# Optimization experiments

Measured on AMD Instinct MI355X. Metric: run time of the kernel, lower is better.

Reference implementation:

```python
import jax, jax.numpy as jnp
import numpy as np

D_MODEL = 512
D_STATE = 16
D_CONV = 4
EXPAND = 2
HEADDIM = 64
D_INNER = EXPAND * D_MODEL            # 1024
NHEADS = D_INNER // HEADDIM           # 16
CONV_DIM = D_INNER + 2 * D_STATE      # 1056 (x, B, C channels)
D_IN_PROJ = 2 * D_INNER + 2 * D_STATE + NHEADS  # 2096
EPS = 1e-5
B_SZ, L_SEQ = 8, 4096


def _mamba_param_keys(prefix):
    return [prefix + n for n in
            ('in_proj', 'conv_w', 'conv_b', 'dt_bias', 'A_log', 'D', 'norm_w', 'out_proj')]


def _make_mamba_params(key, prefix):
    ks = jax.random.split(key, 4)
    s = 0.02
    return {
        prefix + 'in_proj': jax.random.normal(ks[0], (D_IN_PROJ, D_MODEL), jnp.float32) * s,
        prefix + 'conv_w': jax.random.normal(ks[1], (CONV_DIM, D_CONV), jnp.float32) * s,
        prefix + 'conv_b': jnp.zeros((CONV_DIM,), jnp.float32),
        prefix + 'dt_bias': jax.random.normal(ks[2], (NHEADS,), jnp.float32) * 0.1,
        prefix + 'A_log': jnp.log(jnp.arange(1, NHEADS + 1, dtype=jnp.float32)),
        prefix + 'D': jnp.ones((NHEADS,), jnp.float32),
        prefix + 'norm_w': jnp.ones((D_INNER,), jnp.float32),
        prefix + 'out_proj': jax.random.normal(ks[3], (D_MODEL, D_INNER), jnp.float32) * s,
    }


def setup_inputs() -> dict:
    key = jax.random.key(0)
    kx, kf, kb, kp = jax.random.split(key, 4)
    inp = {'x': jax.random.normal(kx, (B_SZ, L_SEQ, D_MODEL), jnp.float32)}
    inp.update(_make_mamba_params(kf, 'f_'))
    inp.update(_make_mamba_params(kb, 'b_'))
    kp1, kp2 = jax.random.split(kp)
    inp['proj_w'] = jax.random.normal(kp1, (D_MODEL, 2 * D_MODEL), jnp.float32) * 0.02
    inp['proj_b'] = jnp.zeros((D_MODEL,), jnp.float32)
    inp['ln_w'] = jnp.ones((D_MODEL,), jnp.float32)
    inp['ln_b'] = jnp.zeros((D_MODEL,), jnp.float32)
    return inp


def mamba2(x, in_proj, conv_w, conv_b, dt_bias, A_log, Dp, norm_w, out_proj):
    """Mamba2 block (ngroups=1): in_proj -> causal depthwise conv -> selective scan -> gated RMSNorm -> out_proj."""
    B, L, _ = x.shape
    zxbcdt = x @ in_proj.T                               # [B,L,2096]
    z = zxbcdt[..., :D_INNER]                            # gate
    xBC = zxbcdt[..., D_INNER:D_INNER + CONV_DIM]
    dt = jax.nn.softplus(zxbcdt[..., D_INNER + CONV_DIM:] + dt_bias)  # [B,L,H]
    # causal depthwise conv over (x, B, C) channels + SiLU
    xp = jnp.pad(xBC, ((0, 0), (D_CONV - 1, 0), (0, 0)))
    conv = conv_b + sum(xp[:, k:k + L, :] * conv_w[:, k] for k in range(D_CONV))
    xBC = jax.nn.silu(conv)
    xs = xBC[..., :D_INNER].reshape(B, L, NHEADS, HEADDIM)  # [B,L,H,P]
    Bm = xBC[..., D_INNER:D_INNER + D_STATE]                # [B,L,N]
    Cm = xBC[..., D_INNER + D_STATE:]                       # [B,L,N]
    A = -jnp.exp(A_log)                                     # [H]
    dA = jnp.exp(dt * A)                                    # [B,L,H]

    def step(h, inp):
        dA_t, dt_t, x_t, B_t, C_t = inp                     # [B,H],[B,H],[B,H,P],[B,N],[B,N]
        h = h * dA_t[..., None, None] + (dt_t[..., None] * x_t)[..., None] * B_t[:, None, None, :]
        y = jnp.einsum('bhpn,bn->bhp', h, C_t)
        return h, y

    h0 = jnp.zeros((B, NHEADS, HEADDIM, D_STATE), x.dtype)
    inps = (dA.transpose(1, 0, 2), dt.transpose(1, 0, 2), xs.transpose(1, 0, 2, 3),
            Bm.transpose(1, 0, 2), Cm.transpose(1, 0, 2))
    _, ys = jax.lax.scan(step, h0, inps)                    # ys: [L,B,H,P]
    y = ys.transpose(1, 0, 2, 3) + Dp[:, None] * xs         # skip connection
    y = y.reshape(B, L, D_INNER)
    # gated RMSNorm (norm_before_gate=False)
    y = y * jax.nn.silu(z)
    y = y * jax.lax.rsqrt(jnp.mean(y * y, axis=-1, keepdims=True) + EPS) * norm_w
    return y @ out_proj.T


def _layer_norm(x, w, b):
    mu = jnp.mean(x, axis=-1, keepdims=True)
    v = jnp.var(x, axis=-1, keepdims=True)
    return (x - mu) * jax.lax.rsqrt(v + EPS) * w + b


def reference(x,
              f_in_proj, f_conv_w, f_conv_b, f_dt_bias, f_A_log, f_D, f_norm_w, f_out_proj,
              b_in_proj, b_conv_w, b_conv_b, b_dt_bias, b_A_log, b_D, b_norm_w, b_out_proj,
              proj_w, proj_b, ln_w, ln_b):
    x_fwd = mamba2(x, f_in_proj, f_conv_w, f_conv_b, f_dt_bias, f_A_log, f_D, f_norm_w, f_out_proj)
    x_bwd = jnp.flip(
        mamba2(jnp.flip(x, axis=1), b_in_proj, b_conv_w, b_conv_b, b_dt_bias, b_A_log, b_D, b_norm_w, b_out_proj),
        axis=1)
    comb = jnp.concatenate([x_fwd, x_bwd], axis=-1)         # [B,L,2D]
    out = comb @ proj_w.T + proj_b                          # dropout is identity (eval / p=0)
    return _layer_norm(x + out, ln_w, ln_b)
```

## Files before the change

### kernel.cpp

```cpp
#include <hip/hip_runtime.h>
#include <hip/hip_bf16.h>
#include <math.h>

typedef __bf16 bf16x8_t __attribute__((ext_vector_type(8)));
typedef float f32x4_t __attribute__((ext_vector_type(4)));
typedef unsigned short u16x8_t __attribute__((ext_vector_type(8)));
typedef unsigned short u16x4_t __attribute__((ext_vector_type(4)));

#define DEV __device__ __forceinline__

DEV float bf2f(unsigned short u) {
    unsigned int v = ((unsigned int)u) << 16;
    return __builtin_bit_cast(float, v);
}
DEV unsigned short f2bf(float f) {
    unsigned int u = __builtin_bit_cast(unsigned int, f);
    u += 0x7fffu + ((u >> 16) & 1u);
    return (unsigned short)(u >> 16);
}

__global__ __launch_bounds__(256) void cvt_k(
    const float* __restrict__ in, unsigned short* __restrict__ out, int n8)
{
    int t = blockIdx.x * 256 + threadIdx.x;
    if (t >= n8) return;
    f32x4_t a = ((const f32x4_t*)in)[t * 2];
    f32x4_t b = ((const f32x4_t*)in)[t * 2 + 1];
    u16x8_t o;
#pragma unroll
    for (int j = 0; j < 4; j++) { o[j] = f2bf(a[j]); o[4 + j] = f2bf(b[j]); }
    ((u16x8_t*)out)[t] = o;
}

template <int NT, bool FLIP_A, bool FLIP_C, bool OUT_F32, bool ADD_BIAS, bool ACCUM>
__global__ __launch_bounds__(256, 2) void gemm_bt(
    const unsigned short* __restrict__ A,
    const unsigned short* __restrict__ W,
    void* __restrict__ Cout,
    const float* __restrict__ bias,
    int N, int K, int ldc, int col_ofs)
{
    __shared__ __attribute__((aligned(16))) unsigned char smem[32768];
    const int tid  = threadIdx.x;
    const int wave = tid >> 6;
    const int lane = tid & 63;

    int mtile_i, ntile_i;
    if (NT == 0) {
        mtile_i = blockIdx.y;
        ntile_i = blockIdx.x;
    } else {
        const int L = blockIdx.x;
        const int MTl = (int)gridDim.x / NT;
        const int ppx = MTl >> 3;
        const int xcd = L & 7, q = L >> 3;
        mtile_i = xcd * ppx + q / NT;
        ntile_i = q % NT;
    }
    const int mtile = mtile_i << 7;
    const int ntile = ntile_i << 7;

    const int c0 = tid, c1 = 256 + tid;
    const int r0 = c0 >> 2, p0 = c0 & 3, g0 = p0 ^ ((r0 >> 1) & 3);
    const int r1 = c1 >> 2, p1 = c1 & 3, g1 = p1 ^ ((r1 >> 1) & 3);

    int am0 = mtile + r0; if (FLIP_A) am0 ^= 4095;
    int am1 = mtile + r1; if (FLIP_A) am1 ^= 4095;
    const unsigned short* aP0 = A + (size_t)am0 * K + g0 * 8;
    const unsigned short* aP1 = A + (size_t)am1 * K + g1 * 8;

    int wr0 = ntile + r0; if (wr0 > N - 1) wr0 = N - 1;
    int wr1 = ntile + r1; if (wr1 > N - 1) wr1 = N - 1;
    const unsigned short* wP0 = W + (size_t)wr0 * K + g0 * 8;
    const unsigned short* wP1 = W + (size_t)wr1 * K + g1 * 8;

    const int stago = wave * 1024;

    f32x4_t acc[4][4] = {};

    const int wm = (wave & 1) << 6;
    const int wn = (wave >> 1) << 6;
    const int r    = lane & 15;
    const int quad = lane >> 4;
    const int sw   = (r >> 1) & 3;

    int aoff[4], woff[4];
#pragma unroll
    for (int i = 0; i < 4; i++) {
        int m = wm + i * 16 + r;
        aoff[i] = (m * 4 + (quad ^ sw)) * 16;
        int n = wn + i * 16 + r;
        woff[i] = (n * 4 + (quad ^ sw)) * 16 + 8192;
    }

    auto STAGE = [&](int kt, int bufsel) {
        const int k0 = kt << 5;
        unsigned char* base = smem + bufsel * 16384;
        __builtin_amdgcn_global_load_lds(
            (const __attribute__((address_space(1))) void*)(aP0 + k0),
            (__attribute__((address_space(3))) void*)(base + stago), 16, 0, 0);
        __builtin_amdgcn_global_load_lds(
            (const __attribute__((address_space(1))) void*)(aP1 + k0),
            (__attribute__((address_space(3))) void*)(base + 4096 + stago), 16, 0, 0);
        __builtin_amdgcn_global_load_lds(
            (const __attribute__((address_space(1))) void*)(wP0 + k0),
            (__attribute__((address_space(3))) void*)(base + 8192 + stago), 16, 0, 0);
        __builtin_amdgcn_global_load_lds(
            (const __attribute__((address_space(1))) void*)(wP1 + k0),
            (__attribute__((address_space(3))) void*)(base + 12288 + stago), 16, 0, 0);
    };

    const int nt = K >> 5;
    STAGE(0, 0);
    __syncthreads();

    for (int kt = 0; kt < nt; kt++) {
        const int cur = kt & 1;
        if (kt + 1 < nt) STAGE(kt + 1, cur ^ 1);

        const unsigned char* bufc = smem + cur * 16384;
        bf16x8_t af[4], wf[4];
#pragma unroll
        for (int i = 0; i < 4; i++)
            af[i] = __builtin_bit_cast(bf16x8_t, *(const u16x8_t*)(bufc + aoff[i]));
#pragma unroll
        for (int j = 0; j < 4; j++)
            wf[j] = __builtin_bit_cast(bf16x8_t, *(const u16x8_t*)(bufc + woff[j]));
#pragma unroll
        for (int i = 0; i < 4; i++)
#pragma unroll
            for (int j = 0; j < 4; j++)
                acc[i][j] = __builtin_amdgcn_mfma_f32_16x16x32_bf16(af[i], wf[j], acc[i][j], 0, 0, 0);
        __syncthreads();
    }

#pragma unroll
    for (int i = 0; i < 4; i++) {
#pragma unroll
        for (int j = 0; j < 4; j++) {
            int cc = ntile + wn + j * 16 + r;
            if (cc >= N) continue;
#pragma unroll
            for (int reg = 0; reg < 4; reg++) {
                int rr = mtile + wm + i * 16 + quad * 4 + reg;
                int orow = FLIP_C ? (rr ^ 4095) : rr;
                float v = acc[i][j][reg];
                if (ADD_BIAS) v += bias[cc];
                if (OUT_F32) {
                    float* p = (float*)Cout + (size_t)orow * ldc + col_ofs + cc;
                    if (ACCUM) v += *p;
                    *p = v;
                } else {
                    ((unsigned short*)Cout)[(size_t)orow * ldc + col_ofs + cc] = f2bf(v);
                }
            }
        }
    }
}

__global__ __launch_bounds__(256) void pack_pw_k(
    const float* __restrict__ pw, unsigned short* __restrict__ pwb)
{
    int t = blockIdx.x * 256 + threadIdx.x;
    int j8 = t & 63;
    int n  = (t >> 6) & 511;
    int dir = t >> 15;
    const float* src = pw + (size_t)n * 1024 + dir * 512 + j8 * 8;
    f32x4_t a = *(const f32x4_t*)src;
    f32x4_t b = *(const f32x4_t*)(src + 4);
    u16x8_t o;
#pragma unroll
    for (int j = 0; j < 4; j++) { o[j] = f2bf(a[j]); o[4 + j] = f2bf(b[j]); }
    *(u16x8_t*)(pwb + (size_t)dir * 512 * 512 + (size_t)n * 512 + j8 * 8) = o;
}

__global__ __launch_bounds__(256) void tr_op_k(
    const float* __restrict__ op0, const float* __restrict__ op1,
    unsigned short* __restrict__ opT)
{
    __shared__ float tile[32][33];
    const int dir = blockIdx.z;
    const float* op = dir ? op1 : op0;
    const int k0 = blockIdx.x * 32;
    const int j0 = blockIdx.y * 32;
    const int tx = threadIdx.x & 31, ty = threadIdx.x >> 5;
#pragma unroll
    for (int i = 0; i < 4; i++) {
        int j = j0 + ty + i * 8;
        tile[ty + i * 8][tx] = op[(size_t)j * 1024 + k0 + tx];
    }
    __syncthreads();
    unsigned short* dst = opT + (size_t)dir * 1024 * 512;
#pragma unroll
    for (int i = 0; i < 4; i++) {
        int k = k0 + ty + i * 8;
        dst[(size_t)k * 512 + j0 + tx] = f2bf(tile[tx][ty + i * 8]);
    }
}

__global__ __launch_bounds__(256) void conv_silu_k(
    const unsigned short* __restrict__ xin,
    const float* __restrict__ cw,
    const float* __restrict__ cb,
    unsigned short* __restrict__ outp)
{
    int t = blockIdx.x * 256 + threadIdx.x;
    int c8 = t % 132;
    int rb = t / 132;
    int c = c8 * 8;
    int row0 = rb * 8;
    int l0 = row0 & 4095;

    float w[8][4];
#pragma unroll
    for (int j = 0; j < 8; j++) {
        f32x4_t wv = *(const f32x4_t*)(cw + (c + j) * 4);
        w[j][0] = wv[0]; w[j][1] = wv[1]; w[j][2] = wv[2]; w[j][3] = wv[3];
    }
    float bia[8];
    {
        f32x4_t b0 = *(const f32x4_t*)(cb + c);
        f32x4_t b1 = *(const f32x4_t*)(cb + c + 4);
#pragma unroll
        for (int j = 0; j < 4; j++) { bia[j] = b0[j]; bia[4 + j] = b1[j]; }
    }

    u16x8_t zero;
#pragma unroll
    for (int j = 0; j < 8; j++) zero[j] = 0;

    u16x8_t win[11];
#pragma unroll
    for (int u = 0; u < 11; u++) {
        int lu = l0 - 3 + u;
        win[u] = (lu >= 0)
            ? *(const u16x8_t*)(xin + (size_t)(row0 - 3 + u) * 1072 + c)
            : zero;
    }

#pragma unroll
    for (int s = 0; s < 8; s++) {
        float acc[8];
#pragma unroll
        for (int j = 0; j < 8; j++) acc[j] = bia[j];
#pragma unroll
        for (int k = 0; k < 4; k++) {
            u16x8_t xv = win[s + k];
#pragma unroll
            for (int j = 0; j < 8; j++)
                acc[j] = fmaf(bf2f(xv[j]), w[j][k], acc[j]);
        }
        u16x8_t o;
#pragma unroll
        for (int j = 0; j < 8; j++) {
            float xx = acc[j];
            o[j] = f2bf(xx * __builtin_amdgcn_rcpf(1.f + __expf(-xx)));
        }
        *(u16x8_t*)(outp + (size_t)(row0 + s) * 1056 + c) = o;
    }
}

__global__ __launch_bounds__(256) void dt_pre_k(
    const unsigned short* __restrict__ xin,
    const float* __restrict__ dt_bias,
    const float* __restrict__ A_log,
    float* __restrict__ dtb, float* __restrict__ ldab)
{
    int t = blockIdx.x * 256 + threadIdx.x;
    int h = t & 15;
    int row = t >> 4;
    float x = bf2f(xin[(size_t)row * 1072 + 1056 + h]) + dt_bias[h];
    float dt = (x > 20.f) ? x : log1pf(__expf(x));
    float A = -__expf(A_log[h]);
    dtb[t] = dt;
    ldab[t] = dt * A;
}

DEV void stage_xt(const unsigned short* __restrict__ xrow, unsigned short* XtW, int l)
{
    u16x8_t xv[8];
#pragma unroll
    for (int m = 0; m < 8; m++) xv[m] = *(const u16x8_t*)(xrow + m * 8);
#pragma unroll
    for (int p = 0; p < 64; p++) {
        int blkc = (l >> 3) ^ (p & 7);
        XtW[p * 64 + blkc * 8 + (l & 7)] = xv[p >> 3][p & 7];
    }
}

DEV bf16x8_t xt_frag(const unsigned short* XtW, int r, int quad, int jj, int kk)
{
    int p = jj * 16 + r;
    int blkc = (kk * 4 + quad) ^ (p & 7);
    return __builtin_bit_cast(bf16x8_t, *(const u16x8_t*)(XtW + p * 64 + blkc * 8));
}

__global__ __launch_bounds__(256) void scan_chstate_k(
    const unsigned short* __restrict__ xc,
    const float* __restrict__ dtb,
    float* __restrict__ lcs,
    float* __restrict__ Hend, float* __restrict__ dec)
{
    __shared__ __attribute__((aligned(16))) unsigned char sm[37120];
    unsigned short* Btr = (unsigned short*)sm;
    float* csW = (float*)(sm + 2304);
    float* dtW = (float*)(sm + 3328);
    unsigned short* Xt0 = (unsigned short*)(sm + 4352);

    const int tid = threadIdx.x;
    const int w = tid >> 6, l = tid & 63;
    const int r = l & 15, quad = l >> 4;
    const int row0 = blockIdx.x * 64;
    const int b = blockIdx.x >> 6, chunk = blockIdx.x & 63;
    const int h = blockIdx.y * 4 + w;
    const int blk = ((b * 16 + h) << 6) | chunk;

    {
        int n = tid & 15, s0 = (tid >> 4) * 4;
#pragma unroll
        for (int js = 0; js < 4; js++) {
            int s = s0 + js;
            Btr[n * 72 + s] = xc[(size_t)(row0 + s) * 1056 + 1024 + n];
        }
    }

    float v   = lcs[(size_t)(row0 + l) * 16 + h];
    float dtv = dtb[(size_t)(row0 + l) * 16 + h];
#pragma unroll
    for (int d = 1; d < 64; d <<= 1) {
        float o = __shfl_up(v, d, 64);
        if (l >= d) v += o;
    }
    lcs[(size_t)(row0 + l) * 16 + h] = v;
    csW[w * 64 + l] = v;
    dtW[w * 64 + l] = dtv;
    if (l == 63) dec[blk] = __expf(v);
    __syncthreads();

    unsigned short* XtW = Xt0 + w * 4096;
    stage_xt(xc + (size_t)(row0 + l) * 1056 + h * 64, XtW, l);

    const float* csr = csW + w * 64;
    const float* dtr = dtW + w * 64;
    float cs63 = csr[63];

    f32x4_t z = {0.f, 0.f, 0.f, 0.f};
    f32x4_t hacc[4] = {z, z, z, z};
#pragma unroll
    for (int kk = 0; kk < 2; kk++) {
        int sb = kk * 32 + quad * 8;
        u16x8_t bv = *(const u16x8_t*)(Btr + r * 72 + sb);
        f32x4_t c0 = *(const f32x4_t*)(csr + sb);
        f32x4_t c1 = *(const f32x4_t*)(csr + sb + 4);
        f32x4_t d0 = *(const f32x4_t*)(dtr + sb);
        f32x4_t d1 = *(const f32x4_t*)(dtr + sb + 4);
        u16x8_t wv;
#pragma unroll
        for (int j = 0; j < 4; j++) {
            wv[j]     = f2bf(bf2f(bv[j])     * d0[j] * __expf(cs63 - c0[j]));
            wv[4 + j] = f2bf(bf2f(bv[4 + j]) * d1[j] * __expf(cs63 - c1[j]));
        }
        bf16x8_t wf = __builtin_bit_cast(bf16x8_t, wv);
#pragma unroll
        for (int jj = 0; jj < 4; jj++)
            hacc[jj] = __builtin_amdgcn_mfma_f32_16x16x32_bf16(wf, xt_frag(XtW, r, quad, jj, kk), hacc[jj], 0, 0, 0);
    }
    float* o = Hend + (size_t)blk * 1024;
#pragma unroll
    for (int jj = 0; jj < 4; jj++)
#pragma unroll
        for (int reg = 0; reg < 4; reg++)
            o[(jj * 16 + r) * 16 + quad * 4 + reg] = hacc[jj][reg];
}

__global__ __launch_bounds__(64) void scan_comb_k(float* __restrict__ H, const float* __restrict__ dec)
{
    int bh = blockIdx.x >> 2;
    int q  = blockIdx.x & 3;
    int t  = threadIdx.x;
    float* base = H + (size_t)bh * 64 * 1024 + q * 256 + t * 4;
    const float* dp = dec + bh * 64;
    f32x4_t hs = {0.f, 0.f, 0.f, 0.f};
    f32x4_t cur = *(const f32x4_t*)base;
    for (int c = 0; c < 64; c++) {
        int cn = (c < 63) ? c + 1 : 63;
        f32x4_t nxt = *(const f32x4_t*)(base + (size_t)cn * 1024);
        float d = dp[c];
        *(f32x4_t*)(base + (size_t)c * 1024) = hs;
#pragma unroll
        for (int j = 0; j < 4; j++) hs[j] = fmaf(hs[j], d, cur[j]);
        cur = nxt;
    }
}

__global__ __launch_bounds__(256) void scan_chout_k(
    const unsigned short* __restrict__ xc,
    const float* __restrict__ dtb, const float* __restrict__ csb,
    const float* __restrict__ Hst, const float* __restrict__ Dp,
    unsigned short* __restrict__ ybuf)
{
    __shared__ __attribute__((aligned(16))) unsigned char sm[60416];
    unsigned short* Ct = (unsigned short*)sm;
    unsigned short* Bt = (unsigned short*)(sm + 4096);
    float* S   = (float*)(sm + 8192);
    float* csL = (float*)(sm + 25600);
    float* dtL = (float*)(sm + 26624);
    unsigned short* Xt0 = (unsigned short*)(sm + 27648);

    const int tid = threadIdx.x;
    const int w = tid >> 6, l = tid & 63;
    const int r = l & 15, quad = l >> 4;
    const int row0 = blockIdx.x * 64;
    const int b = blockIdx.x >> 6, chunk = blockIdx.x & 63;
    const int h = blockIdx.y * 4 + w;
    const int blk = ((b * 16 + h) << 6) | chunk;

    {
        int rowi = tid >> 2, seg = tid & 3;
        u16x8_t vb, vc;
        if (seg < 2) {
            const unsigned short* src = xc + (size_t)(row0 + rowi) * 1056 + 1024 + seg * 8;
            vb = *(const u16x8_t*)src;
            vc = *(const u16x8_t*)(src + 16);
        } else {
#pragma unroll
            for (int j = 0; j < 8; j++) { vb[j] = 0; vc[j] = 0; }
        }
        *(u16x8_t*)(Bt + rowi * 32 + seg * 8) = vb;
        *(u16x8_t*)(Ct + rowi * 32 + seg * 8) = vc;
    }
    csL[w * 64 + l] = csb[(size_t)(row0 + l) * 16 + h];
    dtL[w * 64 + l] = dtb[(size_t)(row0 + l) * 16 + h];
    __syncthreads();

    {
        bf16x8_t cf = __builtin_bit_cast(bf16x8_t, *(const u16x8_t*)(Ct + (w * 16 + r) * 32 + quad * 8));
        f32x4_t z = {0.f, 0.f, 0.f, 0.f};
#pragma unroll
        for (int j = 0; j < 4; j++) {
            bf16x8_t bfv = __builtin_bit_cast(bf16x8_t, *(const u16x8_t*)(Bt + (j * 16 + r) * 32 + quad * 8));
            f32x4_t d = __builtin_amdgcn_mfma_f32_16x16x32_bf16(cf, bfv, z, 0, 0, 0);
#pragma unroll
            for (int reg = 0; reg < 4; reg++)
                S[(w * 16 + quad * 4 + reg) * 68 + j * 16 + r] = d[reg];
        }
    }
    __syncthreads();

    unsigned short* XtW = Xt0 + w * 4096;
    stage_xt(xc + (size_t)(row0 + l) * 1056 + h * 64, XtW, l);

    const float* csr = csL + w * 64;
    const float* dtr = dtL + w * 64;

    f32x4_t acc[4][4];
    {
        bf16x8_t hf[4];
#pragma unroll
        for (int jj = 0; jj < 4; jj++) {
            int p = jj * 16 + r;
            u16x8_t hv;
            if (quad < 2) {
                const float* hp = Hst + (size_t)blk * 1024 + p * 16 + quad * 8;
                f32x4_t h0 = *(const f32x4_t*)hp;
                f32x4_t h1 = *(const f32x4_t*)(hp + 4);
#pragma unroll
                for (int j = 0; j < 4; j++) { hv[j] = f2bf(h0[j]); hv[4 + j] = f2bf(h1[j]); }
            } else {
#pragma unroll
                for (int j = 0; j < 8; j++) hv[j] = 0;
            }
            hf[jj] = __builtin_bit_cast(bf16x8_t, hv);
        }
        f32x4_t z = {0.f, 0.f, 0.f, 0.f};
#pragma unroll
        for (int i = 0; i < 4; i++) {
            bf16x8_t cf = __builtin_bit_cast(bf16x8_t, *(const u16x8_t*)(Ct + (i * 16 + r) * 32 + quad * 8));
#pragma unroll
            for (int jj = 0; jj < 4; jj++)
                acc[i][jj] = __builtin_amdgcn_mfma_f32_16x16x32_bf16(cf, hf[jj], z, 0, 0, 0);
        }
#pragma unroll
        for (int i = 0; i < 4; i++) {
            f32x4_t es;
#pragma unroll
            for (int reg = 0; reg < 4; reg++) es[reg] = __expf(csr[i * 16 + quad * 4 + reg]);
#pragma unroll
            for (int jj = 0; jj < 4; jj++)
#pragma unroll
                for (int reg = 0; reg < 4; reg++) acc[i][jj][reg] *= es[reg];
        }
    }

#pragma unroll
    for (int kk = 0; kk < 2; kk++) {
        int sb = kk * 32 + quad * 8;
        bf16x8_t xf[4];
#pragma unroll
        for (int jj = 0; jj < 4; jj++) xf[jj] = xt_frag(XtW, r, quad, jj, kk);
        f32x4_t c0 = *(const f32x4_t*)(csr + sb);
        f32x4_t c1 = *(const f32x4_t*)(csr + sb + 4);
        f32x4_t d0 = *(const f32x4_t*)(dtr + sb);
        f32x4_t d1 = *(const f32x4_t*)(dtr + sb + 4);
#pragma unroll
        for (int i = 0; i < 4; i++) {
            int t = i * 16 + r;
            float cst = csr[t];
            const float* Srow = S + t * 68;
            f32x4_t s0 = *(const f32x4_t*)(Srow + sb);
            f32x4_t s1 = *(const f32x4_t*)(Srow + sb + 4);
            u16x8_t wv;
#pragma unroll
            for (int j = 0; j < 4; j++) {
                int s = sb + j;
                float v0 = (s <= t) ? __expf(cst - c0[j]) * d0[j] * s0[j] : 0.f;
                wv[j] = f2bf(v0);
                int s2 = sb + 4 + j;
                float v1 = (s2 <= t) ? __expf(cst - c1[j]) * d1[j] * s1[j] : 0.f;
                wv[4 + j] = f2bf(v1);
            }
            bf16x8_t wf = __builtin_bit_cast(bf16x8_t, wv);
#pragma unroll
            for (int jj = 0; jj < 4; jj++)
                acc[i][jj] = __builtin_amdgcn_mfma_f32_16x16x32_bf16(wf, xf[jj], acc[i][jj], 0, 0, 0);
        }
    }

    float Dh = Dp[h];
#pragma unroll
    for (int i = 0; i < 4; i++) {
#pragma unroll
        for (int jj = 0; jj < 4; jj++) {
            int p = jj * 16 + r;
            int t0 = i * 16 + quad * 4;
            int blk2 = (t0 >> 3) ^ (p & 7);
            u16x4_t x4 = *(const u16x4_t*)(XtW + p * 64 + blk2 * 8 + (t0 & 7));
#pragma unroll
            for (int reg = 0; reg < 4; reg++) {
                float yv = fmaf(Dh, bf2f(x4[reg]), acc[i][jj][reg]);
                ybuf[(size_t)(row0 + t0 + reg) * 1024 + h * 64 + p] = f2bf(yv);
            }
        }
    }
}

__global__ __launch_bounds__(256) void rmsgate_k(
    unsigned short* __restrict__ y,
    const unsigned short* __restrict__ z,
    const float* __restrict__ nw)
{
    const int wave = threadIdx.x >> 6, lane = threadIdx.x & 63;
    const size_t row = (size_t)blockIdx.x * 4 + wave;
    const int c = lane * 16;
    unsigned short* yp = y + row * 1024 + c;
    const unsigned short* zp = z + row * 1024 + c;
    u16x8_t yv0 = *(const u16x8_t*)yp;
    u16x8_t yv1 = *(const u16x8_t*)(yp + 8);
    u16x8_t zv0 = *(const u16x8_t*)zp;
    u16x8_t zv1 = *(const u16x8_t*)(zp + 8);
    float g[16];
    float ss = 0.f;
#pragma unroll
    for (int j = 0; j < 8; j++) {
        float zf = bf2f(zv0[j]);
        float sil = zf * __builtin_amdgcn_rcpf(1.f + __expf(-zf));
        g[j] = bf2f(yv0[j]) * sil;
        ss += g[j] * g[j];
    }
#pragma unroll
    for (int j = 0; j < 8; j++) {
        float zf = bf2f(zv1[j]);
        float sil = zf * __builtin_amdgcn_rcpf(1.f + __expf(-zf));
        g[8 + j] = bf2f(yv1[j]) * sil;
        ss += g[8 + j] * g[8 + j];
    }
#pragma unroll
    for (int m = 32; m > 0; m >>= 1) ss += __shfl_xor(ss, m, 64);
    float scale = rsqrtf(ss * (1.f / 1024.f) + 1e-5f);
    f32x4_t w0 = *(const f32x4_t*)(nw + c);
    f32x4_t w1 = *(const f32x4_t*)(nw + c + 4);
    f32x4_t w2 = *(const f32x4_t*)(nw + c + 8);
    f32x4_t w3 = *(const f32x4_t*)(nw + c + 12);
    u16x8_t o0, o1;
#pragma unroll
    for (int j = 0; j < 4; j++) {
        o0[j]     = f2bf(g[j]      * scale * w0[j]);
        o0[4 + j] = f2bf(g[4 + j]  * scale * w1[j]);
        o1[j]     = f2bf(g[8 + j]  * scale * w2[j]);
        o1[4 + j] = f2bf(g[12 + j] * scale * w3[j]);
    }
    *(u16x8_t*)yp = o0;
    *(u16x8_t*)(yp + 8) = o1;
}

__global__ __launch_bounds__(256) void ln_k(
    const float* __restrict__ x,
    const float* __restrict__ f,
    const float* __restrict__ lw,
    const float* __restrict__ lb,
    float* __restrict__ outp)
{
    const int wave = threadIdx.x >> 6, lane = threadIdx.x & 63;
    const size_t row = (size_t)blockIdx.x * 4 + wave;
    const int c = lane * 8;
    f32x4_t xv0 = *(const f32x4_t*)(x + row * 512 + c);
    f32x4_t xv1 = *(const f32x4_t*)(x + row * 512 + c + 4);
    f32x4_t fv0 = *(const f32x4_t*)(f + row * 512 + c);
    f32x4_t fv1 = *(const f32x4_t*)(f + row * 512 + c + 4);
    float s[8];
    float sum = 0.f, sq = 0.f;
#pragma unroll
    for (int j = 0; j < 4; j++) {
        s[j] = xv0[j] + fv0[j];
        s[4 + j] = xv1[j] + fv1[j];
    }
#pragma unroll
    for (int j = 0; j < 8; j++) { sum += s[j]; sq += s[j] * s[j]; }
#pragma unroll
    for (int m = 32; m > 0; m >>= 1) {
        sum += __shfl_xor(sum, m, 64);
        sq  += __shfl_xor(sq, m, 64);
    }
    float mu = sum * (1.f / 512.f);
    float var = sq * (1.f / 512.f) - mu * mu;
    if (var < 0.f) var = 0.f;
    float inv = rsqrtf(var + 1e-5f);
    f32x4_t w0 = *(const f32x4_t*)(lw + c);
    f32x4_t w1 = *(const f32x4_t*)(lw + c + 4);
    f32x4_t b0 = *(const f32x4_t*)(lb + c);
    f32x4_t b1 = *(const f32x4_t*)(lb + c + 4);
    f32x4_t o0, o1;
#pragma unroll
    for (int j = 0; j < 4; j++) {
        o0[j] = (s[j] - mu) * inv * w0[j] + b0[j];
        o1[j] = (s[4 + j] - mu) * inv * w1[j] + b1[j];
    }
    *(f32x4_t*)(outp + row * 512 + c) = o0;
    *(f32x4_t*)(outp + row * 512 + c + 4) = o1;
}

extern "C" void kernel_launch(void* const* d_in, const int* in_sizes, int n_in,
                              void* d_out, int out_size, void* d_ws, size_t ws_size,
                              hipStream_t stream)
{
    (void)in_sizes; (void)n_in; (void)out_size;

    const float* x           = (const float*)d_in[0];
    const float* in_proj[2]  = {(const float*)d_in[1],  (const float*)d_in[9]};
    const float* conv_w[2]   = {(const float*)d_in[2],  (const float*)d_in[10]};
    const float* conv_b[2]   = {(const float*)d_in[3],  (const float*)d_in[11]};
    const float* dt_bias[2]  = {(const float*)d_in[4],  (const float*)d_in[12]};
    const float* A_log[2]    = {(const float*)d_in[5],  (const float*)d_in[13]};
    const float* Dp[2]       = {(const float*)d_in[6],  (const float*)d_in[14]};
    const float* norm_w[2]   = {(const float*)d_in[7],  (const float*)d_in[15]};
    const float* out_proj[2] = {(const float*)d_in[8],  (const float*)d_in[16]};
    const float* proj_w      = (const float*)d_in[17];
    const float* proj_b      = (const float*)d_in[18];
    const float* ln_w        = (const float*)d_in[19];
    const float* ln_b        = (const float*)d_in[20];
    float* outp = (float*)d_out;

    const size_t IP_ELEMS = (size_t)2096 * 512;
    const size_t X_ELEMS  = (size_t)32768 * 512;

    const size_t constBytes = X_ELEMS * 2 + 2 * IP_ELEMS * 2 + 2 * 512 * 1024 * 2
                            + 2 * 512 * 512 * 2 + 2 * 1024 * 512 * 2 + 8192;
    int g = 1;
    {
        const int cands[3] = {8, 4, 2};
        for (int ci = 0; ci < 3; ci++) {
            size_t R = (size_t)cands[ci] * 4096;
            size_t need = constBytes + R * (2144 + 2112 + 2048 + 64 + 64 + 1024)
                        + (size_t)cands[ci] * 1024 * 4 + 16 * 256;
            if (need <= ws_size) { g = cands[ci]; break; }
        }
    }
    const size_t R = (size_t)g * 4096;
    const int nGroups = 8 / g;
    const int MT = (int)(R >> 7);

    char* ws = (char*)d_ws;
    size_t off = 0;
    auto alloc = [&](size_t bytes) -> char* {
        char* p = ws + off;
        off += (bytes + 255) & ~(size_t)255;
        return p;
    };
    unsigned short* xb16  = (unsigned short*)alloc(X_ELEMS * 2);
    unsigned short* ipb16[2];
    ipb16[0] = (unsigned short*)alloc(IP_ELEMS * 2);
    ipb16[1] = (unsigned short*)alloc(IP_ELEMS * 2);
    unsigned short* Ebuf  = (unsigned short*)alloc(2 * 512 * 1024 * 2);
    unsigned short* Ef    = Ebuf;
    unsigned short* Eb    = Ebuf + 512 * 1024;
    unsigned short* pwb   = (unsigned short*)alloc(2 * 512 * 512 * 2);
    unsigned short* opT   = (unsigned short*)alloc(2 * 1024 * 512 * 2);
    unsigned short* xbcdt = (unsigned short*)alloc(R * 1072 * 2);
    unsigned short* ybuf  = xbcdt;
    unsigned short* xconv = (unsigned short*)alloc(R * 1056 * 2);
    unsigned short* zbuf  = xconv;
    float* fbuf = (float*)alloc(R * 512 * 4);
    float* dtb  = (float*)alloc(R * 16 * 4);
    float* dab  = (float*)alloc(R * 16 * 4);
    float* Hbuf = (float*)alloc(R * 1024);
    float* dec  = (float*)alloc((size_t)g * 1024 * 4);

    dim3 blk(256);

    cvt_k<<<(unsigned)((X_ELEMS / 8 + 255) / 256), blk, 0, stream>>>(x, xb16, (int)(X_ELEMS / 8));
    cvt_k<<<(unsigned)((IP_ELEMS / 8 + 255) / 256), blk, 0, stream>>>(in_proj[0], ipb16[0], (int)(IP_ELEMS / 8));
    cvt_k<<<(unsigned)((IP_ELEMS / 8 + 255) / 256), blk, 0, stream>>>(in_proj[1], ipb16[1], (int)(IP_ELEMS / 8));
    pack_pw_k<<<256, blk, 0, stream>>>(proj_w, pwb);
    tr_op_k<<<dim3(32, 16, 2), blk, 0, stream>>>(out_proj[0], out_proj[1], opT);
    gemm_bt<0, false, false, false, false, false><<<dim3(8, 4), blk, 0, stream>>>(
        pwb, opT, Ef, nullptr, 1024, 512, 1024, 0);
    gemm_bt<0, false, false, false, false, false><<<dim3(8, 4), blk, 0, stream>>>(
        pwb + 512 * 512, opT + 1024 * 512, Eb, nullptr, 1024, 512, 1024, 0);

    for (int grp = 0; grp < nGroups; grp++) {
        const unsigned short* xg = xb16 + (size_t)grp * R * 512;
        const float* xgf = x + (size_t)grp * R * 512;
        float* og = outp + (size_t)grp * R * 512;

        for (int dir = 0; dir < 2; dir++) {
            if (dir == 0)
                gemm_bt<9, false, false, false, false, false><<<(unsigned)(9 * MT), blk, 0, stream>>>(
                    xg, ipb16[0] + (size_t)1024 * 512, xbcdt, nullptr, 1072, 512, 1072, 0);
            else
                gemm_bt<9, true, false, false, false, false><<<(unsigned)(9 * MT), blk, 0, stream>>>(
                    xg, ipb16[1] + (size_t)1024 * 512, xbcdt, nullptr, 1072, 512, 1072, 0);

            conv_silu_k<<<(unsigned)(R * 132 / 2048), blk, 0, stream>>>(xbcdt, conv_w[dir], conv_b[dir], xconv);
            dt_pre_k<<<(unsigned)(R * 16 / 256), blk, 0, stream>>>(xbcdt, dt_bias[dir], A_log[dir], dtb, dab);

            scan_chstate_k<<<dim3((unsigned)(R / 64), 4), blk, 0, stream>>>(xconv, dtb, dab, Hbuf, dec);
            scan_comb_k<<<(unsigned)(g * 64), dim3(64), 0, stream>>>(Hbuf, dec);
            scan_chout_k<<<dim3((unsigned)(R / 64), 4), blk, 0, stream>>>(xconv, dtb, dab, Hbuf, Dp[dir], ybuf);

            if (dir == 0)
                gemm_bt<8, false, false, false, false, false><<<(unsigned)(8 * MT), blk, 0, stream>>>(
                    xg, ipb16[0], zbuf, nullptr, 1024, 512, 1024, 0);
            else
                gemm_bt<8, true, false, false, false, false><<<(unsigned)(8 * MT), blk, 0, stream>>>(
                    xg, ipb16[1], zbuf, nullptr, 1024, 512, 1024, 0);

            rmsgate_k<<<(unsigned)(R / 4), blk, 0, stream>>>(ybuf, zbuf, norm_w[dir]);

            if (dir == 0)
                gemm_bt<4, false, false, true, true, false><<<(unsigned)(4 * MT), blk, 0, stream>>>(
                    ybuf, Ef, fbuf, proj_b, 512, 1024, 512, 0);
            else
                gemm_bt<4, false, true, true, false, true><<<(unsigned)(4 * MT), blk, 0, stream>>>(
                    ybuf, Eb, fbuf, nullptr, 512, 1024, 512, 0);
        }
        ln_k<<<(unsigned)(R / 4), blk, 0, stream>>>(xgf, fbuf, ln_w, ln_b, og);
    }
}
```

Before: 876.9 us.

## Merge z and xBCdt in_proj GEMMs into one wide GEMM with strided buffers

The weights are reordered so the xBC/dt rows come first and the z rows follow, and the two separate in_proj GEMMs (1072 and 1024 columns) become one GEMM over 2096 columns into a single row-strided buffer. A lda parameter is added to the GEMM so later stages can read A from that strided buffer. The scan output, the gating kernel and the out-projection GEMM now work in place inside the 2096-wide buffer. This removes one launch and one extra read of the input activations, and gives the GEMM more tiles. In exchange the intermediate buffer grows and accesses become strided, which may cut the group size and cache efficiency.

```diff
diff --git a/kernel.cpp b/kernel.cpp
--- a/kernel.cpp
+++ b/kernel.cpp
@@ -38,7 +38,7 @@
     const unsigned short* __restrict__ W,
     void* __restrict__ Cout,
     const float* __restrict__ bias,
-    int N, int K, int ldc, int col_ofs)
+    int N, int K, int lda, int ldc, int col_ofs)
 {
     __shared__ __attribute__((aligned(16))) unsigned char smem[32768];
     const int tid  = threadIdx.x;
@@ -66,8 +66,8 @@
 
     int am0 = mtile + r0; if (FLIP_A) am0 ^= 4095;
     int am1 = mtile + r1; if (FLIP_A) am1 ^= 4095;
-    const unsigned short* aP0 = A + (size_t)am0 * K + g0 * 8;
-    const unsigned short* aP1 = A + (size_t)am1 * K + g1 * 8;
+    const unsigned short* aP0 = A + (size_t)am0 * lda + g0 * 8;
+    const unsigned short* aP1 = A + (size_t)am1 * lda + g1 * 8;
 
     int wr0 = ntile + r0; if (wr0 > N - 1) wr0 = N - 1;
     int wr1 = ntile + r1; if (wr1 > N - 1) wr1 = N - 1;
@@ -234,7 +234,7 @@
     for (int u = 0; u < 11; u++) {
         int lu = l0 - 3 + u;
         win[u] = (lu >= 0)
-            ? *(const u16x8_t*)(xin + (size_t)(row0 - 3 + u) * 1072 + c)
+            ? *(const u16x8_t*)(xin + (size_t)(row0 - 3 + u) * 2096 + c)
             : zero;
     }
 
@@ -269,7 +269,7 @@
     int t = blockIdx.x * 256 + threadIdx.x;
     int h = t & 15;
     int row = t >> 4;
-    float x = bf2f(xin[(size_t)row * 1072 + 1056 + h]) + dt_bias[h];
+    float x = bf2f(xin[(size_t)row * 2096 + 1056 + h]) + dt_bias[h];
     float dt = (x > 20.f) ? x : log1pf(__expf(x));
     float A = -__expf(A_log[h]);
     dtb[t] = dt;
@@ -538,7 +538,7 @@
 #pragma unroll
             for (int reg = 0; reg < 4; reg++) {
                 float yv = fmaf(Dh, bf2f(x4[reg]), acc[i][jj][reg]);
-                ybuf[(size_t)(row0 + t0 + reg) * 1024 + h * 64 + p] = f2bf(yv);
+                ybuf[(size_t)(row0 + t0 + reg) * 2096 + h * 64 + p] = f2bf(yv);
             }
         }
     }
@@ -552,8 +552,8 @@
     const int wave = threadIdx.x >> 6, lane = threadIdx.x & 63;
     const size_t row = (size_t)blockIdx.x * 4 + wave;
     const int c = lane * 16;
-    unsigned short* yp = y + row * 1024 + c;
-    const unsigned short* zp = z + row * 1024 + c;
+    unsigned short* yp = y + row * 2096 + c;
+    const unsigned short* zp = z + row * 2096 + c;
     u16x8_t yv0 = *(const u16x8_t*)yp;
     u16x8_t yv1 = *(const u16x8_t*)(yp + 8);
     u16x8_t zv0 = *(const u16x8_t*)zp;
@@ -670,7 +670,7 @@
         const int cands[3] = {8, 4, 2};
         for (int ci = 0; ci < 3; ci++) {
             size_t R = (size_t)cands[ci] * 4096;
-            size_t need = constBytes + R * (2144 + 2112 + 2048 + 64 + 64 + 1024)
+            size_t need = constBytes + R * (4192 + 2112 + 2048 + 64 + 64 + 1024)
                         + (size_t)cands[ci] * 1024 * 4 + 16 * 256;
             if (need <= ws_size) { g = cands[ci]; break; }
         }
@@ -695,10 +695,8 @@
     unsigned short* Eb    = Ebuf + 512 * 1024;
     unsigned short* pwb   = (unsigned short*)alloc(2 * 512 * 512 * 2);
     unsigned short* opT   = (unsigned short*)alloc(2 * 1024 * 512 * 2);
-    unsigned short* xbcdt = (unsigned short*)alloc(R * 1072 * 2);
-    unsigned short* ybuf  = xbcdt;
+    unsigned short* xbcdt = (unsigned short*)alloc(R * 2096 * 2);
     unsigned short* xconv = (unsigned short*)alloc(R * 1056 * 2);
-    unsigned short* zbuf  = xconv;
     float* fbuf = (float*)alloc(R * 512 * 4);
     float* dtb  = (float*)alloc(R * 16 * 4);
     float* dab  = (float*)alloc(R * 16 * 4);
@@ -708,14 +706,18 @@
     dim3 blk(256);
 
     cvt_k<<<(unsigned)((X_ELEMS / 8 + 255) / 256), blk, 0, stream>>>(x, xb16, (int)(X_ELEMS / 8));
-    cvt_k<<<(unsigned)((IP_ELEMS / 8 + 255) / 256), blk, 0, stream>>>(in_proj[0], ipb16[0], (int)(IP_ELEMS / 8));
-    cvt_k<<<(unsigned)((IP_ELEMS / 8 + 255) / 256), blk, 0, stream>>>(in_proj[1], ipb16[1], (int)(IP_ELEMS / 8));
+    for (int d = 0; d < 2; d++) {
+        cvt_k<<<(unsigned)((1072 * 512 / 8 + 255) / 256), blk, 0, stream>>>(
+            in_proj[d] + (size_t)1024 * 512, ipb16[d], 1072 * 512 / 8);
+        cvt_k<<<(unsigned)((1024 * 512 / 8 + 255) / 256), blk, 0, stream>>>(
+            in_proj[d], ipb16[d] + (size_t)1072 * 512, 1024 * 512 / 8);
+    }
     pack_pw_k<<<256, blk, 0, stream>>>(proj_w, pwb);
     tr_op_k<<<dim3(32, 16, 2), blk, 0, stream>>>(out_proj[0], out_proj[1], opT);
     gemm_bt<0, false, false, false, false, false><<<dim3(8, 4), blk, 0, stream>>>(
-        pwb, opT, Ef, nullptr, 1024, 512, 1024, 0);
+        pwb, opT, Ef, nullptr, 1024, 512, 512, 1024, 0);
     gemm_bt<0, false, false, false, false, false><<<dim3(8, 4), blk, 0, stream>>>(
-        pwb + 512 * 512, opT + 1024 * 512, Eb, nullptr, 1024, 512, 1024, 0);
+        pwb + 512 * 512, opT + 1024 * 512, Eb, nullptr, 1024, 512, 512, 1024, 0);
 
     for (int grp = 0; grp < nGroups; grp++) {
         const unsigned short* xg = xb16 + (size_t)grp * R * 512;
@@ -724,34 +726,27 @@
 
         for (int dir = 0; dir < 2; dir++) {
             if (dir == 0)
-                gemm_bt<9, false, false, false, false, false><<<(unsigned)(9 * MT), blk, 0, stream>>>(
-                    xg, ipb16[0] + (size_t)1024 * 512, xbcdt, nullptr, 1072, 512, 1072, 0);
+                gemm_bt<17, false, false, false, false, false><<<(unsigned)(17 * MT), blk, 0, stream>>>(
+                    xg, ipb16[0], xbcdt, nullptr, 2096, 512, 512, 2096, 0);
             else
-                gemm_bt<9, true, false, false, false, false><<<(unsigned)(9 * MT), blk, 0, stream>>>(
-                    xg, ipb16[1] + (size_t)1024 * 512, xbcdt, nullptr, 1072, 512, 1072, 0);
+                gemm_bt<17, true, false, false, false, false><<<(unsigned)(17 * MT), blk, 0, stream>>>(
+                    xg, ipb16[1], xbcdt, nullptr, 2096, 512, 512, 2096, 0);
 
             conv_silu_k<<<(unsigned)(R * 132 / 2048), blk, 0, stream>>>(xbcdt, conv_w[dir], conv_b[dir], xconv);
             dt_pre_k<<<(unsigned)(R * 16 / 256), blk, 0, stream>>>(xbcdt, dt_bias[dir], A_log[dir], dtb, dab);
 
             scan_chstate_k<<<dim3((unsigned)(R / 64), 4), blk, 0, stream>>>(xconv, dtb, dab, Hbuf, dec);
             scan_comb_k<<<(unsigned)(g * 64), dim3(64), 0, stream>>>(Hbuf, dec);
-            scan_chout_k<<<dim3((unsigned)(R / 64), 4), blk, 0, stream>>>(xconv, dtb, dab, Hbuf, Dp[dir], ybuf);
-
-            if (dir == 0)
-                gemm_bt<8, false, false, false, false, false><<<(unsigned)(8 * MT), blk, 0, stream>>>(
-                    xg, ipb16[0], zbuf, nullptr, 1024, 512, 1024, 0);
-            else
-                gemm_bt<8, true, false, false, false, false><<<(unsigned)(8 * MT), blk, 0, stream>>>(
-                    xg, ipb16[1], zbuf, nullptr, 1024, 512, 1024, 0);
-
-            rmsgate_k<<<(unsigned)(R / 4), blk, 0, stream>>>(ybuf, zbuf, norm_w[dir]);
+            scan_chout_k<<<dim3((unsigned)(R / 64), 4), blk, 0, stream>>>(xconv, dtb, dab, Hbuf, Dp[dir], xbcdt);
+
+            rmsgate_k<<<(unsigned)(R / 4), blk, 0, stream>>>(xbcdt, xbcdt + 1072, norm_w[dir]);
 
             if (dir == 0)
                 gemm_bt<4, false, false, true, true, false><<<(unsigned)(4 * MT), blk, 0, stream>>>(
-                    ybuf, Ef, fbuf, proj_b, 512, 1024, 512, 0);
+                    xbcdt, Ef, fbuf, proj_b, 512, 1024, 2096, 512, 0);
             else
                 gemm_bt<4, false, true, true, false, true><<<(unsigned)(4 * MT), blk, 0, stream>>>(
-                    ybuf, Eb, fbuf, nullptr, 512, 1024, 512, 0);
+                    xbcdt, Eb, fbuf, nullptr, 512, 1024, 2096, 512, 0);
         }
         ln_k<<<(unsigned)(R / 4), blk, 0, stream>>>(xgf, fbuf, ln_w, ln_b, og);
     }
```

Result: no change. 888.0 us (+1.3%).
